# Optimization experiments

Measured on AMD Instinct MI355X. Metric: run time of the kernel, lower is better.

The kernel has to match this reference:

```python
import jax, jax.numpy as jnp
import numpy as np

B, T, H, V, L = 16, 256, 512, 32, 2


def setup_inputs() -> dict:
    key = jax.random.key(0)
    ks = jax.random.split(key, 24)
    s = 1.0 / np.sqrt(H)
    d = {}
    d["encoder_outputs"] = jax.random.normal(ks[0], (B, T, H), jnp.float32)
    d["h0"] = jax.random.normal(ks[1], (L, B, H), jnp.float32)
    d["c0"] = jax.random.normal(ks[2], (L, B, H), jnp.float32)
    d["audio_lengths"] = jax.random.randint(ks[3], (B,), 1, T + 1, jnp.int32)
    d["Wq"] = jax.random.normal(ks[4], (H, H), jnp.float32) * s
    d["bq"] = jnp.zeros((H,), jnp.float32)
    d["Wk"] = jax.random.normal(ks[5], (H, H), jnp.float32) * s
    d["bk"] = jnp.zeros((H,), jnp.float32)
    d["v"] = jax.random.normal(ks[6], (H,), jnp.float32) * s
    d["vb"] = jnp.zeros((1,), jnp.float32)
    d["Wih0"] = jax.random.normal(ks[7], (4 * H, 2 * H), jnp.float32) * s
    d["bih0"] = jnp.zeros((4 * H,), jnp.float32)
    d["Whh0"] = jax.random.normal(ks[8], (4 * H, H), jnp.float32) * s
    d["bhh0"] = jnp.zeros((4 * H,), jnp.float32)
    d["Wih1"] = jax.random.normal(ks[9], (4 * H, H), jnp.float32) * s
    d["bih1"] = jnp.zeros((4 * H,), jnp.float32)
    d["Whh1"] = jax.random.normal(ks[10], (4 * H, H), jnp.float32) * s
    d["bhh1"] = jnp.zeros((4 * H,), jnp.float32)
    d["Wout"] = jax.random.normal(ks[11], (V, H), jnp.float32) * s
    d["bout"] = jnp.zeros((V,), jnp.float32)
    return d


def _lstm_cell(x, h, c, Wih, bih, Whh, bhh):
    # PyTorch gate order: i, f, g, o
    g = x @ Wih.T + bih + h @ Whh.T + bhh
    i, f, gg, o = jnp.split(g, 4, axis=-1)
    c2 = jax.nn.sigmoid(f) * c + jax.nn.sigmoid(i) * jnp.tanh(gg)
    h2 = jax.nn.sigmoid(o) * jnp.tanh(c2)
    return h2, c2


def reference(encoder_outputs, h0, c0, audio_lengths, Wq, bq, Wk, bk, v, vb,
              Wih0, bih0, Whh0, bhh0, Wih1, bih1, Whh1, bhh1, Wout, bout):
    # Precompute key projection once (same math as per-step Wk @ keys)
    Kproj = encoder_outputs @ Wk.T + bk  # [B,T,H]

    def step(carry, enc_t):
        h, c = carry  # each [L,B,H]
        q = h[-1]  # [B,H] top-layer hidden drives attention
        e = jnp.tanh((q @ Wq.T + bq)[:, None, :] + Kproj)  # [B,T,H]
        scores = jnp.einsum('bth,h->bt', e, v) + vb[0]  # [B,T]
        w = jax.nn.softmax(scores, axis=-1)
        ctx = jnp.einsum('bt,bth->bh', w, encoder_outputs)  # [B,H]
        x = jnp.concatenate([enc_t, ctx], axis=-1)  # [B,2H]
        h0n, c0n = _lstm_cell(x, h[0], c[0], Wih0, bih0, Whh0, bhh0)
        h1n, c1n = _lstm_cell(h0n, h[1], c[1], Wih1, bih1, Whh1, bhh1)
        logit = h1n @ Wout.T + bout  # [B,V]
        return (jnp.stack([h0n, h1n]), jnp.stack([c0n, c1n])), logit

    _, logits = jax.lax.scan(step, (h0, c0), jnp.swapaxes(encoder_outputs, 0, 1))
    return jnp.swapaxes(logits, 0, 1)  # [B,T,V]
```

## Files before the change

### kernel.cpp

```cpp
#include <hip/hip_runtime.h>

#define HH 512
#define BB 16
#define TT 256
#define VV 32
#define TPB 512
#define NBLK 256
#define PITCH 516

#define BAR_INTS 512

struct KArgs {
  const float* enc; const float* h0in; const float* c0in;
  const float* Wq; const float* bq; const float* vatt; const float* vb;
  const float* Wih0; const float* bih0; const float* Whh0; const float* bhh0;
  const float* Wih1; const float* bih1; const float* Whh1; const float* bhh1;
  const float* Wout; const float* bout;
  const float* Kproj; float* H0buf; float* H1buf; float* qWg; float* Ug; float* Zg;
  int* bar; float* out;
};

struct Smem {
  float W0e[4][2][PITCH];
  float W0c[4][2][PITCH];
  float W0h[4][2][PITCH];
  float W1x[4][2][PITCH];
  float W1h[4][2][PITCH];
  float Wqr[2][PITCH];
  float Wor[2][PITCH];
  float vv[HH];
  union { float qrow[HH]; float red[8][64]; } qr;
  float stg[BB][PITCH];
  float pre0[BB][4][2];
  float pre1[BB][4][2];
  float cst[2][2][BB];
  float scw[16];
  float zinv[BB];
  float bs0[4][2];
  float bs1[4][2];
  float bqv[2], boutv[2];
};

__device__ __forceinline__ float fsig(float x){ return 1.0f/(1.0f + __expf(-x)); }
__device__ __forceinline__ float ftanh(float x){
  float ee = __expf(2.0f*x);
  return 1.0f - 2.0f/(ee + 1.0f);
}

__device__ __forceinline__ void stcc(float* p, float v){
  __hip_atomic_store(p, v, __ATOMIC_RELAXED, __HIP_MEMORY_SCOPE_AGENT);
}
__device__ __forceinline__ float ldcc(const float* p){
  return __hip_atomic_load(p, __ATOMIC_RELAXED, __HIP_MEMORY_SCOPE_AGENT);
}
__device__ __forceinline__ float2 ld2cc(const float* p){
  unsigned long long v = __hip_atomic_load((const unsigned long long*)p,
                                           __ATOMIC_RELAXED, __HIP_MEMORY_SCOPE_AGENT);
  union { unsigned long long u; float2 f; } c; c.u = v;
  return c.f;
}

__device__ __forceinline__ void ldbuf_cc(const float* __restrict__ src,
                                         float2* __restrict__ v, int tid){
  #pragma unroll
  for (int it = 0; it < 8; ++it)
    v[it] = ld2cc(&src[(it*TPB + tid)*2]);
}
__device__ __forceinline__ void stg_regs(const float2* __restrict__ v,
                                         float (* __restrict__ stg)[PITCH], int tid){
  #pragma unroll
  for (int it = 0; it < 8; ++it){
    const int i2 = (it*TPB + tid)*2;
    *(float2*)&stg[i2 >> 9][i2 & 511] = v[it];
  }
}

__device__ __forceinline__ void gbar_arrive(int* __restrict__ bar, int e, int bid){
  __syncthreads();
  if (threadIdx.x == 0)
    __hip_atomic_store(&bar[bid], e, __ATOMIC_RELAXED, __HIP_MEMORY_SCOPE_AGENT);
}
__device__ __forceinline__ void gbar_wait(int* __restrict__ bar, int e, int bid){
  if (threadIdx.x < 64){
    const unsigned long long* p = (const unsigned long long*)bar;
    const int i0 = threadIdx.x * 2;
    int spins = 0;
    for (;;){
      unsigned long long v0 = __hip_atomic_load(&p[i0],     __ATOMIC_RELAXED, __HIP_MEMORY_SCOPE_AGENT);
      unsigned long long v1 = __hip_atomic_load(&p[i0 + 1], __ATOMIC_RELAXED, __HIP_MEMORY_SCOPE_AGENT);
      const int a0 = (int)v0, a1 = (int)(v0 >> 32), a2 = (int)v1, a3 = (int)(v1 >> 32);
      const int ok = (a0 >= e) & (a1 >= e) & (a2 >= e) & (a3 >= e);
      if (__all(ok)) break;
      __builtin_amdgcn_s_sleep(2);
      if (++spins > (1 << 20)) break;
    }
  }
  __syncthreads();
}

__device__ __forceinline__ void gbar2(int* __restrict__ bar2, int et, int bid, int ba){
  __syncthreads();
  if (threadIdx.x == 0)
    __hip_atomic_store(&bar2[bid], et, __ATOMIC_RELAXED, __HIP_MEMORY_SCOPE_AGENT);
  if (threadIdx.x < 64){
    const unsigned long long* p = (const unsigned long long*)bar2 + ba*8;
    int spins = 0;
    for (;;){
      int ok = 1;
      if (threadIdx.x < 8){
        unsigned long long v = __hip_atomic_load(&p[threadIdx.x], __ATOMIC_RELAXED, __HIP_MEMORY_SCOPE_AGENT);
        ok = ((int)v >= et) & ((int)(v >> 32) >= et);
      }
      if (__all(ok)) break;
      __builtin_amdgcn_s_sleep(1);
      if (++spins > (1 << 20)) break;
    }
  }
  __syncthreads();
}

__device__ __forceinline__ void dot8(const float* __restrict__ W,
                                     const float (* __restrict__ stg)[PITCH],
                                     float (* __restrict__ red)[64],
                                     int wave, int lane){
  const int jj = wave >> 2, off = (wave & 3) << 7;
  const int b = lane & 15, g = lane >> 4;
  const float* wrow = W + (size_t)(g*2 + jj)*PITCH + off;
  const float* xrow = &stg[b][off];
  float a0 = 0.f, a1 = 0.f, a2 = 0.f, a3 = 0.f;
  #pragma unroll
  for (int h = 0; h < 128; h += 16){
    const float4 w0 = *(const float4*)&wrow[h];      const float4 x0 = *(const float4*)&xrow[h];
    const float4 w1 = *(const float4*)&wrow[h + 4];  const float4 x1 = *(const float4*)&xrow[h + 4];
    const float4 w2 = *(const float4*)&wrow[h + 8];  const float4 x2 = *(const float4*)&xrow[h + 8];
    const float4 w3 = *(const float4*)&wrow[h + 12]; const float4 x3 = *(const float4*)&xrow[h + 12];
    a0 = fmaf(w0.x,x0.x, fmaf(w0.y,x0.y, fmaf(w0.z,x0.z, fmaf(w0.w,x0.w, a0))));
    a1 = fmaf(w1.x,x1.x, fmaf(w1.y,x1.y, fmaf(w1.z,x1.z, fmaf(w1.w,x1.w, a1))));
    a2 = fmaf(w2.x,x2.x, fmaf(w2.y,x2.y, fmaf(w2.z,x2.z, fmaf(w2.w,x2.w, a2))));
    a3 = fmaf(w3.x,x3.x, fmaf(w3.y,x3.y, fmaf(w3.z,x3.z, fmaf(w3.w,x3.w, a3))));
  }
  red[wave][lane] = (a0 + a1) + (a2 + a3);
}

__global__ void init_kernel(const float* __restrict__ h0in, float* __restrict__ H0buf,
                            float* __restrict__ H1buf, float* __restrict__ Ug,
                            float* __restrict__ Zg, int* __restrict__ bar){
  const int i = blockIdx.x*blockDim.x + threadIdx.x;
  if (i < BB*HH){
    H0buf[i] = h0in[i];
    H1buf[i] = h0in[BB*HH + i];
  }
  if (i < 2*BB*HH) Ug[i] = 0.0f;
  if (i < 32) Zg[i] = 0.0f;
  if (i < BAR_INTS) bar[i] = 0;
}

__global__ __launch_bounds__(256, 1) void kproj_kernel(const float* __restrict__ enc,
                                                       const float* __restrict__ Wk,
                                                       const float* __restrict__ bk,
                                                       float* __restrict__ Kproj){
  __shared__ float er[BB][PITCH];
  const int bid = blockIdx.x, tid = threadIdx.x;
  const int wave = tid >> 6, lane = tid & 63;
  const int r = lane & 15, q = lane >> 4;
  const int row0 = bid*16;
  #pragma unroll
  for (int it = 0; it < 8; ++it){
    const int idx = (it*256 + tid)*4;
    const int rr = idx >> 9, h = idx & 511;
    *(float4*)&er[rr][h] = *(const float4*)&enc[(size_t)(row0+rr)*HH + h];
  }
  __syncthreads();
  float4 xr[32];
  #pragma unroll
  for (int i = 0; i < 32; ++i) xr[i] = *(const float4*)&er[r][q*128 + i*4];
  for (int k = 0; k < 128; ++k){
    const int hk = wave*128 + k;
    const float* wrow = Wk + (size_t)hk*HH + q*128;
    float acc = 0.f;
    #pragma unroll
    for (int i = 0; i < 32; ++i){
      const float4 w4 = *(const float4*)&wrow[i*4];
      acc = fmaf(w4.x,xr[i].x, fmaf(w4.y,xr[i].y, fmaf(w4.z,xr[i].z, fmaf(w4.w,xr[i].w, acc))));
    }
    acc += __shfl_xor(acc, 16);
    acc += __shfl_xor(acc, 32);
    if (lane < 16) Kproj[(size_t)(row0 + r)*HH + hk] = acc + bk[hk];
  }
}

__global__ __launch_bounds__(TPB, 1) void decoder_persist(KArgs a){
  __shared__ Smem S;
  const int bid = blockIdx.x, tid = threadIdx.x;
  const int wave = tid >> 6, lane = tid & 63;
  const int lb = lane & 15, lg = lane >> 4;
  const int j0 = bid*2;
  const int ba = bid >> 4, tb = (bid & 15) * 16;
  int* bar2 = a.bar + 256;

  for (int g = 0; g < 4; ++g){
    for (int jj = 0; jj < 2; ++jj){
      const int row = g*HH + j0 + jj;
      for (int h = tid; h < HH; h += TPB){
        S.W0e[g][jj][h] = a.Wih0[(size_t)row*(2*HH) + h];
        S.W0c[g][jj][h] = a.Wih0[(size_t)row*(2*HH) + HH + h];
        S.W0h[g][jj][h] = a.Whh0[(size_t)row*HH + h];
        S.W1x[g][jj][h] = a.Wih1[(size_t)row*HH + h];
        S.W1h[g][jj][h] = a.Whh1[(size_t)row*HH + h];
      }
    }
  }
  for (int jj = 0; jj < 2; ++jj){
    const int d = bid*2 + jj, vo = d & 31;
    for (int h = tid; h < HH; h += TPB){
      S.Wqr[jj][h] = a.Wq[(size_t)(j0+jj)*HH + h];
      S.Wor[jj][h] = a.Wout[(size_t)vo*HH + h];
    }
  }
  for (int h = tid; h < HH; h += TPB) S.vv[h] = a.vatt[h];
  if (tid < 16){
    S.cst[0][0][tid] = a.c0in[0*BB*HH + tid*HH + j0];
    S.cst[0][1][tid] = a.c0in[0*BB*HH + tid*HH + j0 + 1];
    S.cst[1][0][tid] = a.c0in[1*BB*HH + tid*HH + j0];
    S.cst[1][1][tid] = a.c0in[1*BB*HH + tid*HH + j0 + 1];
  }
  if (tid < 8){
    const int g = tid & 3, jj = tid >> 2;
    const int row = g*HH + j0 + jj;
    S.bs0[g][jj] = a.bih0[row] + a.bhh0[row];
    S.bs1[g][jj] = a.bih1[row] + a.bhh1[row];
  }
  if (tid < 2){
    S.bqv[tid] = a.bq[j0 + tid];
    S.boutv[tid] = a.bout[(bid*2 + tid) & 31];
  }
  const float vb0 = a.vb[0];

  float r_kp[2][8];
  #pragma unroll
  for (int i = 0; i < 2; ++i){
    const float* kp = a.Kproj + (size_t)(ba*TT + tb + wave*2 + i)*HH;
    #pragma unroll
    for (int k = 0; k < 8; ++k) r_kp[i][k] = kp[lane + 64*k];
  }
  float r_e[16];
  #pragma unroll
  for (int lt = 0; lt < 16; ++lt)
    r_e[lt] = a.enc[(size_t)(ba*TT + tb + lt)*HH + tid];
  float4 r_en[4];
  #pragma unroll
  for (int it = 0; it < 4; ++it){
    const int idx = (it*TPB + tid)*4;
    r_en[it] = *(const float4*)&a.enc[(size_t)((idx >> 9)*TT + 0)*HH + (idx & 511)];
  }
  __syncthreads();

  {
    #pragma unroll
    for (int it = 0; it < 4; ++it){
      const int idx = (it*TPB + tid)*4;
      *(float4*)&S.stg[idx >> 9][idx & 511] = *(const float4*)&a.h0in[idx];
    }
    __syncthreads();
    dot8(&S.W0h[0][0][0], S.stg, S.qr.red, wave, lane);
    __syncthreads();
    if (tid < 128){
      const int jj = tid >> 6, l = tid & 63, g = l >> 4, b = l & 15;
      S.pre0[b][g][jj] = (S.qr.red[jj*4+0][l] + S.qr.red[jj*4+1][l])
                       + (S.qr.red[jj*4+2][l] + S.qr.red[jj*4+3][l]) + S.bs0[g][jj];
    }
    __syncthreads();
  }

  int e = 0;
  for (int t = 0; t < TT; ++t){
    const int par = t & 1, parn = par ^ 1;

    float2 r_h1[8];
    ldbuf_cc(a.H1buf + par*(BB*HH), r_h1, tid);
    stg_regs(r_h1, S.stg, tid);
    __syncthreads();

    if (wave < 2){
      if (t > 0){
        const int d = bid*2 + wave, bo = d >> 5, vo = d & 31;
        float acc = 0.f;
        #pragma unroll
        for (int k = 0; k < 8; ++k){
          const int h = lane + 64*k;
          acc = fmaf(S.Wor[wave][h], S.stg[bo][h], acc);
        }
        #pragma unroll
        for (int off = 32; off; off >>= 1) acc += __shfl_xor(acc, off);
        if (lane == 0) a.out[(size_t)(bo*TT + (t-1))*VV + vo] = acc + S.boutv[wave];
      }
    } else if (wave < 4){
      const int jj = wave - 2;
      const int off0 = lg * 128;
      float a0 = 0.f, a1 = 0.f;
      #pragma unroll
      for (int h = 0; h < 128; h += 8){
        const float4 w0 = *(const float4*)&S.Wqr[jj][off0 + h];
        const float4 x0 = *(const float4*)&S.stg[lb][off0 + h];
        const float4 w1 = *(const float4*)&S.Wqr[jj][off0 + h + 4];
        const float4 x1 = *(const float4*)&S.stg[lb][off0 + h + 4];
        a0 = fmaf(w0.x,x0.x, fmaf(w0.y,x0.y, fmaf(w0.z,x0.z, fmaf(w0.w,x0.w, a0))));
        a1 = fmaf(w1.x,x1.x, fmaf(w1.y,x1.y, fmaf(w1.z,x1.z, fmaf(w1.w,x1.w, a1))));
      }
      float acc = a0 + a1;
      acc += __shfl_xor(acc, 16);
      acc += __shfl_xor(acc, 32);
      if (lane < 16) stcc(&a.qWg[lane*HH + j0 + jj], acc + S.bqv[jj]);
    }

    e++; gbar_arrive(a.bar, e, bid);

    dot8(&S.W1h[0][0][0], S.stg, S.qr.red, wave, lane);
    __syncthreads();
    if (tid < 128){
      const int jj = tid >> 6, l = tid & 63, g = l >> 4, b = l & 15;
      S.pre1[b][g][jj] = (S.qr.red[jj*4+0][l] + S.qr.red[jj*4+1][l])
                       + (S.qr.red[jj*4+2][l] + S.qr.red[jj*4+3][l]) + S.bs1[g][jj];
    }
    #pragma unroll
    for (int it = 0; it < 4; ++it){
      const int idx = (it*TPB + tid)*4;
      *(float4*)&S.stg[idx >> 9][idx & 511] = r_en[it];
    }
    __syncthreads();
    dot8(&S.W0e[0][0][0], S.stg, S.qr.red, wave, lane);
    __syncthreads();
    if (tid < 128){
      const int jj = tid >> 6, l = tid & 63, g = l >> 4, b = l & 15;
      S.pre0[b][g][jj] += (S.qr.red[jj*4+0][l] + S.qr.red[jj*4+1][l])
                        + (S.qr.red[jj*4+2][l] + S.qr.red[jj*4+3][l]);
    }

    gbar_wait(a.bar, e, bid);

    {
      float* Up = a.Ug + par*(BB*HH);
      float* Zp = a.Zg + par*16;
      const float qv = ldcc(&a.qWg[ba*HH + tid]);
      S.qr.qrow[tid] = qv;
      __syncthreads();
      #pragma unroll
      for (int i = 0; i < 2; ++i){
        float acc = 0.f;
        #pragma unroll
        for (int k = 0; k < 8; ++k){
          const int h = lane + 64*k;
          acc = fmaf(S.vv[h], ftanh(S.qr.qrow[h] + r_kp[i][k]), acc);
        }
        #pragma unroll
        for (int off = 32; off; off >>= 1) acc += __shfl_xor(acc, off);
        if (lane == 0) S.scw[wave*2 + i] = __expf(acc + vb0);
      }
      __syncthreads();
      float u = 0.f;
      #pragma unroll
      for (int lt = 0; lt < 16; ++lt)
        u = fmaf(S.scw[lt], r_e[lt], u);
      unsafeAtomicAdd(&Up[ba*HH + tid], u);
      if (tid == 0){
        float zs = 0.f;
        #pragma unroll
        for (int lt = 0; lt < 16; ++lt) zs += S.scw[lt];
        unsafeAtomicAdd(&Zp[ba], zs);
      }
    }
    gbar2(bar2, t + 1, bid, ba);

    {
      float2 r_u[8];
      ldbuf_cc(a.Ug + par*(BB*HH), r_u, tid);
      if (tid < 16) S.zinv[tid] = 1.0f / ldcc(&a.Zg[par*16 + tid]);
      stg_regs(r_u, S.stg, tid);
      __syncthreads();
      dot8(&S.W0c[0][0][0], S.stg, S.qr.red, wave, lane);
      __syncthreads();
      if (tid < 32){
        const int b = tid & 15, jj = tid >> 4;
        const float zi = S.zinv[b];
        float gv[4];
        #pragma unroll
        for (int g = 0; g < 4; ++g){
          const int l = g*16 + b;
          gv[g] = S.pre0[b][g][jj]
                + ((S.qr.red[jj*4+0][l] + S.qr.red[jj*4+1][l])
                 + (S.qr.red[jj*4+2][l] + S.qr.red[jj*4+3][l])) * zi;
        }
        const float cold = S.cst[0][jj][b];
        const float ii = fsig(gv[0]), ff = fsig(gv[1]);
        const float gg = ftanh(gv[2]), oo = fsig(gv[3]);
        const float cn = ff*cold + ii*gg;
        S.cst[0][jj][b] = cn;
        stcc(&a.H0buf[parn*(BB*HH) + b*HH + j0 + jj], oo * ftanh(cn));
      }
    }
    e++; gbar_arrive(a.bar, e, bid);
    {
      const int tn = (t + 1 < TT) ? (t + 1) : t;
      #pragma unroll
      for (int it = 0; it < 4; ++it){
        const int idx = (it*TPB + tid)*4;
        r_en[it] = *(const float4*)&a.enc[(size_t)((idx >> 9)*TT + tn)*HH + (idx & 511)];
      }
    }
    gbar_wait(a.bar, e, bid);

    {
      if (tid < 32) stcc(&a.Ug[parn*(BB*HH) + bid*32 + tid], 0.0f);
      if (bid == 0 && tid < 16) stcc(&a.Zg[parn*16 + tid], 0.0f);

      float2 r_x[8];
      ldbuf_cc(a.H0buf + parn*(BB*HH), r_x, tid);
      stg_regs(r_x, S.stg, tid);
      __syncthreads();
      dot8(&S.W1x[0][0][0], S.stg, S.qr.red, wave, lane);
      __syncthreads();
      if (tid < 32){
        const int b = tid & 15, jj = tid >> 4;
        float gv[4];
        #pragma unroll
        for (int g = 0; g < 4; ++g){
          const int l = g*16 + b;
          gv[g] = S.pre1[b][g][jj]
                + (S.qr.red[jj*4+0][l] + S.qr.red[jj*4+1][l])
                + (S.qr.red[jj*4+2][l] + S.qr.red[jj*4+3][l]);
        }
        const float cold = S.cst[1][jj][b];
        const float ii = fsig(gv[0]), ff = fsig(gv[1]);
        const float gg = ftanh(gv[2]), oo = fsig(gv[3]);
        const float cn = ff*cold + ii*gg;
        S.cst[1][jj][b] = cn;
        stcc(&a.H1buf[parn*(BB*HH) + b*HH + j0 + jj], oo * ftanh(cn));
      }
    }
    e++; gbar_arrive(a.bar, e, bid);
    {
      dot8(&S.W0h[0][0][0], S.stg, S.qr.red, wave, lane);
      __syncthreads();
      if (tid < 128){
        const int jj = tid >> 6, l = tid & 63, g = l >> 4, b = l & 15;
        S.pre0[b][g][jj] = (S.qr.red[jj*4+0][l] + S.qr.red[jj*4+1][l])
                         + (S.qr.red[jj*4+2][l] + S.qr.red[jj*4+3][l]) + S.bs0[g][jj];
      }
    }
    gbar_wait(a.bar, e, bid);
  }

  {
    float2 r_x[8];
    ldbuf_cc(a.H1buf, r_x, tid);
    stg_regs(r_x, S.stg, tid);
    __syncthreads();
    if (wave < 2){
      const int d = bid*2 + wave, bo = d >> 5, vo = d & 31;
      float acc = 0.f;
      #pragma unroll
      for (int k = 0; k < 8; ++k){
        const int h = lane + 64*k;
        acc = fmaf(S.Wor[wave][h], S.stg[bo][h], acc);
      }
      #pragma unroll
      for (int off = 32; off; off >>= 1) acc += __shfl_xor(acc, off);
      if (lane == 0) a.out[(size_t)(bo*TT + 255)*VV + vo] = acc + S.boutv[wave];
    }
  }
}

extern "C" void kernel_launch(void* const* d_in, const int* in_sizes, int n_in,
                              void* d_out, int out_size, void* d_ws, size_t ws_size,
                              hipStream_t stream){
  const float* enc  = (const float*)d_in[0];
  const float* h0in = (const float*)d_in[1];
  const float* c0in = (const float*)d_in[2];
  const float* Wq   = (const float*)d_in[4];
  const float* bq   = (const float*)d_in[5];
  const float* Wk   = (const float*)d_in[6];
  const float* bk   = (const float*)d_in[7];
  const float* vatt = (const float*)d_in[8];
  const float* vb   = (const float*)d_in[9];
  const float* Wih0 = (const float*)d_in[10];
  const float* bih0 = (const float*)d_in[11];
  const float* Whh0 = (const float*)d_in[12];
  const float* bhh0 = (const float*)d_in[13];
  const float* Wih1 = (const float*)d_in[14];
  const float* bih1 = (const float*)d_in[15];
  const float* Whh1 = (const float*)d_in[16];
  const float* bhh1 = (const float*)d_in[17];
  const float* Wout = (const float*)d_in[18];
  const float* bout = (const float*)d_in[19];

  float* ws    = (float*)d_ws;
  float* Kproj = ws;
  float* H0buf = Kproj + (size_t)BB*TT*HH;
  float* H1buf = H0buf + 2*BB*HH;
  float* qWg   = H1buf + 2*BB*HH;
  float* Ug    = qWg + BB*HH;
  float* Zg    = Ug + 2*BB*HH;
  int*   bar   = (int*)(Zg + 32);

  hipLaunchKernelGGL(init_kernel, dim3(64), dim3(256), 0, stream,
                     h0in, H0buf, H1buf, Ug, Zg, bar);
  hipLaunchKernelGGL(kproj_kernel, dim3(256), dim3(256), 0, stream, enc, Wk, bk, Kproj);

  KArgs ka;
  ka.enc = enc; ka.h0in = h0in; ka.c0in = c0in;
  ka.Wq = Wq; ka.bq = bq; ka.vatt = vatt; ka.vb = vb;
  ka.Wih0 = Wih0; ka.bih0 = bih0; ka.Whh0 = Whh0; ka.bhh0 = bhh0;
  ka.Wih1 = Wih1; ka.bih1 = bih1; ka.Whh1 = Whh1; ka.bhh1 = bhh1;
  ka.Wout = Wout; ka.bout = bout;
  ka.Kproj = Kproj; ka.H0buf = H0buf; ka.H1buf = H1buf;
  ka.qWg = qWg; ka.Ug = Ug; ka.Zg = Zg; ka.bar = bar; ka.out = (float*)d_out;

  void* params[] = { (void*)&ka };
  hipLaunchCooperativeKernel((const void*)decoder_persist, dim3(NBLK), dim3(TPB),
                             params, 0, stream);
}
```

Measured before the change: 4.705 ms.

## Replace two grid barriers per step with tagged value-flag polling

Removes two of the grid-wide barriers per timestep. Consumers of the q-projection and the layer-0 hidden state now poll 64-bit slots that pack each value with its timestep tag. Each block waits only for the data it reads, instead of all 256 blocks arriving. This trades barrier latency for doubled storage and wider polling loads on H0 (16 loads per thread), and drops the H0 double buffer in favour of the tags. The barrier sleep interval is also shortened.

Measured after the change: 5.845 ms. 1.24x slower.

```diff
diff --git a/kernel.cpp b/kernel.cpp
--- a/kernel.cpp
+++ b/kernel.cpp
@@ -10,13 +10,15 @@
 
 #define BAR_INTS 512
 
+typedef unsigned long long ull;
+
 struct KArgs {
   const float* enc; const float* h0in; const float* c0in;
   const float* Wq; const float* bq; const float* vatt; const float* vb;
   const float* Wih0; const float* bih0; const float* Whh0; const float* bhh0;
   const float* Wih1; const float* bih1; const float* Whh1; const float* bhh1;
   const float* Wout; const float* bout;
-  const float* Kproj; float* H0buf; float* H1buf; float* qWg; float* Ug; float* Zg;
+  const float* Kproj; ull* H0tag; float* H1buf; ull* qWtag; float* Ug; float* Zg;
   int* bar; float* out;
 };
 
@@ -54,10 +56,21 @@
   return __hip_atomic_load(p, __ATOMIC_RELAXED, __HIP_MEMORY_SCOPE_AGENT);
 }
 __device__ __forceinline__ float2 ld2cc(const float* p){
-  unsigned long long v = __hip_atomic_load((const unsigned long long*)p,
-                                           __ATOMIC_RELAXED, __HIP_MEMORY_SCOPE_AGENT);
-  union { unsigned long long u; float2 f; } c; c.u = v;
+  ull v = __hip_atomic_load((const ull*)p, __ATOMIC_RELAXED, __HIP_MEMORY_SCOPE_AGENT);
+  union { ull u; float2 f; } c; c.u = v;
   return c.f;
+}
+
+__device__ __forceinline__ ull  ppack(float v, int tag){
+  return (ull)(unsigned)__float_as_int(v) | ((ull)(unsigned)tag << 32);
+}
+__device__ __forceinline__ float pval(ull x){ return __int_as_float((int)(unsigned)x); }
+__device__ __forceinline__ int   ptag(ull x){ return (int)(unsigned)(x >> 32); }
+__device__ __forceinline__ void st_pair(ull* p, float v, int tag){
+  __hip_atomic_store(p, ppack(v, tag), __ATOMIC_RELAXED, __HIP_MEMORY_SCOPE_AGENT);
+}
+__device__ __forceinline__ ull ld_pair(const ull* p){
+  return __hip_atomic_load(p, __ATOMIC_RELAXED, __HIP_MEMORY_SCOPE_AGENT);
 }
 
 __device__ __forceinline__ void ldbuf_cc(const float* __restrict__ src,
@@ -72,6 +85,24 @@
   for (int it = 0; it < 8; ++it){
     const int i2 = (it*TPB + tid)*2;
     *(float2*)&stg[i2 >> 9][i2 & 511] = v[it];
+  }
+}
+
+__device__ __forceinline__ void poll_stage16(const ull* __restrict__ r, int exptag,
+                                             float (* __restrict__ stg)[PITCH], int tid){
+  int spins = 0;
+  for (;;){
+    int ok = 1;
+    #pragma unroll
+    for (int it = 0; it < 16; ++it){
+      const int idx = it*TPB + tid;
+      const ull v = ld_pair(&r[idx]);
+      ok &= (ptag(v) == exptag);
+      stg[idx >> 9][idx & 511] = pval(v);
+    }
+    if (ok) break;
+    __builtin_amdgcn_s_sleep(1);
+    if (++spins > (1 << 20)) break;
   }
 }
 
@@ -82,16 +113,16 @@
 }
 __device__ __forceinline__ void gbar_wait(int* __restrict__ bar, int e, int bid){
   if (threadIdx.x < 64){
-    const unsigned long long* p = (const unsigned long long*)bar;
+    const ull* p = (const ull*)bar;
     const int i0 = threadIdx.x * 2;
     int spins = 0;
     for (;;){
-      unsigned long long v0 = __hip_atomic_load(&p[i0],     __ATOMIC_RELAXED, __HIP_MEMORY_SCOPE_AGENT);
-      unsigned long long v1 = __hip_atomic_load(&p[i0 + 1], __ATOMIC_RELAXED, __HIP_MEMORY_SCOPE_AGENT);
+      ull v0 = __hip_atomic_load(&p[i0],     __ATOMIC_RELAXED, __HIP_MEMORY_SCOPE_AGENT);
+      ull v1 = __hip_atomic_load(&p[i0 + 1], __ATOMIC_RELAXED, __HIP_MEMORY_SCOPE_AGENT);
       const int a0 = (int)v0, a1 = (int)(v0 >> 32), a2 = (int)v1, a3 = (int)(v1 >> 32);
       const int ok = (a0 >= e) & (a1 >= e) & (a2 >= e) & (a3 >= e);
       if (__all(ok)) break;
-      __builtin_amdgcn_s_sleep(2);
+      __builtin_amdgcn_s_sleep(1);
       if (++spins > (1 << 20)) break;
     }
   }
@@ -103,12 +134,12 @@
   if (threadIdx.x == 0)
     __hip_atomic_store(&bar2[bid], et, __ATOMIC_RELAXED, __HIP_MEMORY_SCOPE_AGENT);
   if (threadIdx.x < 64){
-    const unsigned long long* p = (const unsigned long long*)bar2 + ba*8;
+    const ull* p = (const ull*)bar2 + ba*8;
     int spins = 0;
     for (;;){
       int ok = 1;
       if (threadIdx.x < 8){
-        unsigned long long v = __hip_atomic_load(&p[threadIdx.x], __ATOMIC_RELAXED, __HIP_MEMORY_SCOPE_AGENT);
+        ull v = __hip_atomic_load(&p[threadIdx.x], __ATOMIC_RELAXED, __HIP_MEMORY_SCOPE_AGENT);
         ok = ((int)v >= et) & ((int)(v >> 32) >= et);
       }
       if (__all(ok)) break;
@@ -142,13 +173,15 @@
   red[wave][lane] = (a0 + a1) + (a2 + a3);
 }
 
-__global__ void init_kernel(const float* __restrict__ h0in, float* __restrict__ H0buf,
-                            float* __restrict__ H1buf, float* __restrict__ Ug,
-                            float* __restrict__ Zg, int* __restrict__ bar){
+__global__ void init_kernel(const float* __restrict__ h0in, ull* __restrict__ H0tag,
+                            float* __restrict__ H1buf, ull* __restrict__ qWtag,
+                            float* __restrict__ Ug, float* __restrict__ Zg,
+                            int* __restrict__ bar){
   const int i = blockIdx.x*blockDim.x + threadIdx.x;
   if (i < BB*HH){
-    H0buf[i] = h0in[i];
+    H0tag[i] = ppack(h0in[i], 0);
     H1buf[i] = h0in[BB*HH + i];
+    qWtag[i] = ppack(0.f, 0);
   }
   if (i < 2*BB*HH) Ug[i] = 0.0f;
   if (i < 32) Zg[i] = 0.0f;
@@ -310,10 +343,9 @@
       float acc = a0 + a1;
       acc += __shfl_xor(acc, 16);
       acc += __shfl_xor(acc, 32);
-      if (lane < 16) stcc(&a.qWg[lane*HH + j0 + jj], acc + S.bqv[jj]);
-    }
-
-    e++; gbar_arrive(a.bar, e, bid);
+      if (lane < 16)
+        st_pair(&a.qWtag[lane*HH + j0 + jj], acc + S.bqv[jj], t + 1);
+    }
 
     dot8(&S.W1h[0][0][0], S.stg, S.qr.red, wave, lane);
     __syncthreads();
@@ -335,14 +367,21 @@
       S.pre0[b][g][jj] += (S.qr.red[jj*4+0][l] + S.qr.red[jj*4+1][l])
                         + (S.qr.red[jj*4+2][l] + S.qr.red[jj*4+3][l]);
     }
-
-    gbar_wait(a.bar, e, bid);
+    __syncthreads();
 
     {
       float* Up = a.Ug + par*(BB*HH);
       float* Zp = a.Zg + par*16;
-      const float qv = ldcc(&a.qWg[ba*HH + tid]);
-      S.qr.qrow[tid] = qv;
+      {
+        const ull* q = a.qWtag + ba*HH;
+        int spins = 0;
+        for (;;){
+          const ull v = ld_pair(&q[tid]);
+          if (ptag(v) == t + 1){ S.qr.qrow[tid] = pval(v); break; }
+          __builtin_amdgcn_s_sleep(1);
+          if (++spins > (1 << 20)) break;
+        }
+      }
       __syncthreads();
       #pragma unroll
       for (int i = 0; i < 2; ++i){
@@ -395,10 +434,10 @@
         const float gg = ftanh(gv[2]), oo = fsig(gv[3]);
         const float cn = ff*cold + ii*gg;
         S.cst[0][jj][b] = cn;
-        stcc(&a.H0buf[parn*(BB*HH) + b*HH + j0 + jj], oo * ftanh(cn));
-      }
-    }
-    e++; gbar_arrive(a.bar, e, bid);
+        st_pair(&a.H0tag[b*HH + j0 + jj], oo * ftanh(cn), t + 1);
+      }
+    }
+
     {
       const int tn = (t + 1 < TT) ? (t + 1) : t;
       #pragma unroll
@@ -407,15 +446,12 @@
         r_en[it] = *(const float4*)&a.enc[(size_t)((idx >> 9)*TT + tn)*HH + (idx & 511)];
       }
     }
-    gbar_wait(a.bar, e, bid);
 
     {
       if (tid < 32) stcc(&a.Ug[parn*(BB*HH) + bid*32 + tid], 0.0f);
       if (bid == 0 && tid < 16) stcc(&a.Zg[parn*16 + tid], 0.0f);
 
-      float2 r_x[8];
-      ldbuf_cc(a.H0buf + parn*(BB*HH), r_x, tid);
-      stg_regs(r_x, S.stg, tid);
+      poll_stage16(a.H0tag, t + 1, S.stg, tid);
       __syncthreads();
       dot8(&S.W1x[0][0][0], S.stg, S.qr.red, wave, lane);
       __syncthreads();
@@ -495,15 +531,15 @@
 
   float* ws    = (float*)d_ws;
   float* Kproj = ws;
-  float* H0buf = Kproj + (size_t)BB*TT*HH;
-  float* H1buf = H0buf + 2*BB*HH;
-  float* qWg   = H1buf + 2*BB*HH;
-  float* Ug    = qWg + BB*HH;
+  ull*   H0tag = (ull*)(Kproj + (size_t)BB*TT*HH);
+  float* H1buf = (float*)(H0tag + BB*HH);
+  ull*   qWtag = (ull*)(H1buf + 2*BB*HH);
+  float* Ug    = (float*)(qWtag + BB*HH);
   float* Zg    = Ug + 2*BB*HH;
   int*   bar   = (int*)(Zg + 32);
 
   hipLaunchKernelGGL(init_kernel, dim3(64), dim3(256), 0, stream,
-                     h0in, H0buf, H1buf, Ug, Zg, bar);
+                     h0in, H0tag, H1buf, qWtag, Ug, Zg, bar);
   hipLaunchKernelGGL(kproj_kernel, dim3(256), dim3(256), 0, stream, enc, Wk, bk, Kproj);
 
   KArgs ka;
@@ -512,8 +548,8 @@
   ka.Wih0 = Wih0; ka.bih0 = bih0; ka.Whh0 = Whh0; ka.bhh0 = bhh0;
   ka.Wih1 = Wih1; ka.bih1 = bih1; ka.Whh1 = Whh1; ka.bhh1 = bhh1;
   ka.Wout = Wout; ka.bout = bout;
-  ka.Kproj = Kproj; ka.H0buf = H0buf; ka.H1buf = H1buf;
-  ka.qWg = qWg; ka.Ug = Ug; ka.Zg = Zg; ka.bar = bar; ka.out = (float*)d_out;
+  ka.Kproj = Kproj; ka.H0tag = H0tag; ka.H1buf = H1buf; ka.qWtag = qWtag;
+  ka.Ug = Ug; ka.Zg = Zg; ka.bar = bar; ka.out = (float*)d_out;
 
   void* params[] = { (void*)&ka };
   hipLaunchCooperativeKernel((const void*)decoder_persist, dim3(NBLK), dim3(TPB),
```
